# Kernel optimization log

Hardware: AMD Instinct MI355X
Metric: run time of the kernel (lower is better)

## Reference

```python
import jax, jax.numpy as jnp
import numpy as np

M, K, N = 65536, 512, 512
EPS = 1e-05


def setup_inputs() -> dict:
    key = jax.random.key(0)
    k1, k2, k3 = jax.random.split(key, 3)
    x = jax.random.normal(k1, (M, K), dtype=jnp.float32)
    # int8 weight buffer in [-128, 127]
    weight_int8 = jax.random.randint(k2, (N, K), -128, 128, dtype=jnp.int32).astype(jnp.int8)
    # realistic per-output-channel dequant scales (max-abs / 127 of an fp weight)
    weight_scale = jax.random.uniform(k3, (N,), dtype=jnp.float32, minval=0.001, maxval=0.02)
    return {"x": x, "weight_int8": weight_int8, "weight_scale": weight_scale}


def reference(x, weight_int8, weight_scale):
    # dynamic per-tensor quantization of the activation
    x_scale = jnp.maximum(jnp.max(jnp.abs(x)) / 127.0, EPS)
    x_int8 = jnp.clip(jnp.round(x / x_scale), -128, 127).astype(jnp.int8)
    out_int32 = jnp.matmul(x_int8, weight_int8.T, preferred_element_type=jnp.int32)
    # dequantize: per-tensor input scale * per-row weight scale
    out = out_int32.astype(jnp.float32) * (x_scale * weight_scale[None, :])
    return out
```

## Files before the change

### kernel.cpp

```cpp
#include <hip/hip_runtime.h>


#define M_DIM 65536
#define K_DIM 512
#define N_DIM 512
#define EPSF  1e-5f

typedef int int32x4 __attribute__((ext_vector_type(4)));

#define WS_PART   256
#define WS_WPACK  32768

__device__ inline unsigned int pack_w4(int4 v) {
    return (v.x & 0xff) | ((v.y & 0xff) << 8) |
           ((v.z & 0xff) << 16) | ((unsigned)v.w << 24);
}

__device__ inline unsigned int quantpack4(float4 f, float inv) {
    const float C = 12582912.0f;
    unsigned int u0 = __float_as_uint(fmaf(f.x, inv, C));
    unsigned int u1 = __float_as_uint(fmaf(f.y, inv, C));
    unsigned int u2 = __float_as_uint(fmaf(f.z, inv, C));
    unsigned int u3 = __float_as_uint(fmaf(f.w, inv, C));
    unsigned int lo = __builtin_amdgcn_perm(u1, u0, 0x0C0C0400u);
    unsigned int hi = __builtin_amdgcn_perm(u3, u2, 0x04000C0Cu);
    return lo | hi;
}

__global__ void absmax1_pack_kernel(const float* __restrict__ x,
                                    const int* __restrict__ wi,
                                    float* __restrict__ partials,
                                    unsigned int* __restrict__ wp) {
    const int b = blockIdx.x;
    const int t = threadIdx.x;
    if (b < 4096) {
        __shared__ float red[4];
        const float4* x4 = (const float4*)x;
        const int base = b * 2048;
        float m = 0.0f;
        #pragma unroll
        for (int j = 0; j < 8; ++j) {
            float4 v = x4[base + j * 256 + t];
            m = fmaxf(m, fmaxf(fmaxf(fabsf(v.x), fabsf(v.y)),
                               fmaxf(fabsf(v.z), fabsf(v.w))));
        }
        #pragma unroll
        for (int off = 32; off > 0; off >>= 1)
            m = fmaxf(m, __shfl_xor(m, off));
        if ((t & 63) == 0) red[t >> 6] = m;
        __syncthreads();
        if (t == 0)
            partials[b] = fmaxf(fmaxf(red[0], red[1]), fmaxf(red[2], red[3]));
    } else {
        const int bb = b - 4096;
        #pragma unroll
        for (int j = 0; j < 4; ++j) {
            int d = bb * 1024 + j * 256 + t;
            wp[d] = pack_w4(((const int4*)wi)[d]);
        }
    }
}

__global__ __launch_bounds__(256, 4) void quant_gemm_kernel(
    const float* __restrict__ x, const signed char* __restrict__ w,
    const float* __restrict__ wscale, const float* __restrict__ partials,
    float* __restrict__ out) {
    __shared__ __attribute__((aligned(16))) signed char Blds[32 * 1024];
    __shared__ float red[4];

    const int t    = threadIdx.x;
    const int wave = t >> 6;
    const int lane = t & 63;
    const int quad = lane >> 4;
    const int l16  = lane & 15;
    const int m0   = blockIdx.x * 64;
    const int mw   = m0 + wave * 16;

    #pragma unroll
    for (int cc = 0; cc < 2; ++cc) {
        int c = wave * 2 + cc;
        #pragma unroll
        for (int tt = 0; tt < 4; ++tt) {
            const signed char* g = w + (long)(tt * 16 + l16) * K_DIM
                                     + c * 64 + quad * 16;
            __builtin_amdgcn_global_load_lds(
                (const __attribute__((address_space(1))) unsigned int*)g,
                (__attribute__((address_space(3))) unsigned int*)(Blds + (c * 4 + tt) * 1024),
                16, 0, 0);
        }
    }

    float m = 0.0f;
    {
        const float4* p4 = (const float4*)partials;
        #pragma unroll
        for (int j = 0; j < 4; ++j) {
            float4 v = p4[t + j * 256];
            m = fmaxf(m, fmaxf(fmaxf(v.x, v.y), fmaxf(v.z, v.w)));
        }
        #pragma unroll
        for (int off = 32; off > 0; off >>= 1)
            m = fmaxf(m, __shfl_xor(m, off));
        if (lane == 0) red[wave] = m;
    }
    __syncthreads();
    const float mx  = fmaxf(fmaxf(red[0], red[1]), fmaxf(red[2], red[3]));
    const float s   = fmaxf(mx / 127.0f, EPSF);
    const float inv = 1.0f / s;

    int32x4 a[8];
    {
        const float* xr = x + (size_t)(mw + l16) * K_DIM + quad * 16;
        #pragma unroll
        for (int k = 0; k < 8; ++k) {
            float4 v0 = *(const float4*)(xr + k * 64 + 0);
            float4 v1 = *(const float4*)(xr + k * 64 + 4);
            float4 v2 = *(const float4*)(xr + k * 64 + 8);
            float4 v3 = *(const float4*)(xr + k * 64 + 12);
            a[k].x = (int)quantpack4(v0, inv);
            a[k].y = (int)quantpack4(v1, inv);
            a[k].z = (int)quantpack4(v2, inv);
            a[k].w = (int)quantpack4(v3, inv);
        }
    }

    for (int bx = 0; bx < 8; ++bx) {
        const int n0 = bx * 64;
        __syncthreads();

        int32x4 acc[4] = {};
        #pragma unroll
        for (int k = 0; k < 8; ++k) {
            const signed char* bbase = Blds + k * 4096 + lane * 16;
            #pragma unroll
            for (int tt = 0; tt < 4; ++tt) {
                int32x4 bf = *(const int32x4*)(bbase + tt * 1024);
                acc[tt] = __builtin_amdgcn_mfma_i32_16x16x64_i8(a[k], bf, acc[tt], 0, 0, 0);
            }
        }
        __syncthreads();

        if (bx < 7) {
            const int n1 = (bx + 1) * 64;
            #pragma unroll
            for (int cc = 0; cc < 2; ++cc) {
                int c = wave * 2 + cc;
                #pragma unroll
                for (int tt = 0; tt < 4; ++tt) {
                    const signed char* g = w + (long)(n1 + tt * 16 + l16) * K_DIM
                                             + c * 64 + quad * 16;
                    __builtin_amdgcn_global_load_lds(
                        (const __attribute__((address_space(1))) unsigned int*)g,
                        (__attribute__((address_space(3))) unsigned int*)(Blds + (c * 4 + tt) * 1024),
                        16, 0, 0);
                }
            }
        }

        #pragma unroll
        for (int tt = 0; tt < 4; ++tt) {
            int n = n0 + tt * 16 + l16;
            float c = s * wscale[n];
            float* o = out + (long)(mw + quad * 4) * N_DIM + n;
            #pragma unroll
            for (int r = 0; r < 4; ++r)
                o[(long)r * N_DIM] = (float)acc[tt][r] * c;
        }
    }
}

extern "C" void kernel_launch(void* const* d_in, const int* in_sizes, int n_in,
                              void* d_out, int out_size, void* d_ws, size_t ws_size,
                              hipStream_t stream) {
    const float* x   = (const float*)d_in[0];
    const int*   wi  = (const int*)d_in[1];
    const float* sc  = (const float*)d_in[2];
    float*       out = (float*)d_out;

    float*        partials = (float*)((char*)d_ws + WS_PART);
    unsigned int* wp       = (unsigned int*)((char*)d_ws + WS_WPACK);
    const signed char* w8  = (const signed char*)wp;

    absmax1_pack_kernel<<<4160, 256, 0, stream>>>(x, wi, partials, wp);
    quant_gemm_kernel<<<1024, 256, 0, stream>>>(x, w8, sc, partials, out);
}
```

Before: 279.9 us.

## Stage quantized activation tile through swizzled LDS with coalesced x loads

Activation loads become fully contiguous per block: each thread reads 64 consecutive bytes of the 64x512 x tile, quantizes them, and writes int8 into XOR-swizzled LDS. Each wave then reads its MFMA A fragments back from LDS. Before, each lane read 64 bytes from rows strided by 2 KB. The LDS buffer is reused for weights afterward, so the first weight prefetch now starts only after activation staging, losing the overlap it had with the x loads. Two extra barriers are added.

Measured after the change: 274.9 us. About the same (-1.8%).

```diff
diff --git a/kernel.cpp b/kernel.cpp
--- a/kernel.cpp
+++ b/kernel.cpp
@@ -65,7 +65,7 @@
     const float* __restrict__ x, const signed char* __restrict__ w,
     const float* __restrict__ wscale, const float* __restrict__ partials,
     float* __restrict__ out) {
-    __shared__ __attribute__((aligned(16))) signed char Blds[32 * 1024];
+    __shared__ __attribute__((aligned(16))) signed char Lds[32 * 1024];
     __shared__ float red[4];
 
     const int t    = threadIdx.x;
@@ -76,6 +76,58 @@
     const int m0   = blockIdx.x * 64;
     const int mw   = m0 + wave * 16;
 
+    float m = 0.0f;
+    {
+        const float4* p4 = (const float4*)partials;
+        #pragma unroll
+        for (int j = 0; j < 4; ++j) {
+            float4 v = p4[t + j * 256];
+            m = fmaxf(m, fmaxf(fmaxf(v.x, v.y), fmaxf(v.z, v.w)));
+        }
+        #pragma unroll
+        for (int off = 32; off > 0; off >>= 1)
+            m = fmaxf(m, __shfl_xor(m, off));
+        if (lane == 0) red[wave] = m;
+    }
+    __syncthreads();
+    const float mx  = fmaxf(fmaxf(red[0], red[1]), fmaxf(red[2], red[3]));
+    const float s   = fmaxf(mx / 127.0f, EPSF);
+    const float inv = 1.0f / s;
+
+    {
+        const float4* xs = (const float4*)(x + (size_t)m0 * K_DIM);
+        const int rsub = t >> 5;
+        const int csub = (t & 31) * 16;
+        #pragma unroll
+        for (int j = 0; j < 8; ++j) {
+            const int fi = j * 1024 + t * 4;
+            float4 v0 = xs[fi + 0];
+            float4 v1 = xs[fi + 1];
+            float4 v2 = xs[fi + 2];
+            float4 v3 = xs[fi + 3];
+            int32x4 p;
+            p.x = (int)quantpack4(v0, inv);
+            p.y = (int)quantpack4(v1, inv);
+            p.z = (int)quantpack4(v2, inv);
+            p.w = (int)quantpack4(v3, inv);
+            const int row  = j * 8 + rsub;
+            const int addr = (row * 512 + csub) ^ ((row & 7) << 4);
+            *(int32x4*)(Lds + addr) = p;
+        }
+    }
+    __syncthreads();
+
+    int32x4 a[8];
+    {
+        const int r = wave * 16 + l16;
+        #pragma unroll
+        for (int k = 0; k < 8; ++k) {
+            const int c = quad * 16 + k * 64;
+            a[k] = *(const int32x4*)(Lds + ((r * 512 + c) ^ ((r & 7) << 4)));
+        }
+    }
+    __syncthreads();
+
     #pragma unroll
     for (int cc = 0; cc < 2; ++cc) {
         int c = wave * 2 + cc;
@@ -85,42 +137,8 @@
                                      + c * 64 + quad * 16;
             __builtin_amdgcn_global_load_lds(
                 (const __attribute__((address_space(1))) unsigned int*)g,
-                (__attribute__((address_space(3))) unsigned int*)(Blds + (c * 4 + tt) * 1024),
+                (__attribute__((address_space(3))) unsigned int*)(Lds + (c * 4 + tt) * 1024),
                 16, 0, 0);
-        }
-    }
-
-    float m = 0.0f;
-    {
-        const float4* p4 = (const float4*)partials;
-        #pragma unroll
-        for (int j = 0; j < 4; ++j) {
-            float4 v = p4[t + j * 256];
-            m = fmaxf(m, fmaxf(fmaxf(v.x, v.y), fmaxf(v.z, v.w)));
-        }
-        #pragma unroll
-        for (int off = 32; off > 0; off >>= 1)
-            m = fmaxf(m, __shfl_xor(m, off));
-        if (lane == 0) red[wave] = m;
-    }
-    __syncthreads();
-    const float mx  = fmaxf(fmaxf(red[0], red[1]), fmaxf(red[2], red[3]));
-    const float s   = fmaxf(mx / 127.0f, EPSF);
-    const float inv = 1.0f / s;
-
-    int32x4 a[8];
-    {
-        const float* xr = x + (size_t)(mw + l16) * K_DIM + quad * 16;
-        #pragma unroll
-        for (int k = 0; k < 8; ++k) {
-            float4 v0 = *(const float4*)(xr + k * 64 + 0);
-            float4 v1 = *(const float4*)(xr + k * 64 + 4);
-            float4 v2 = *(const float4*)(xr + k * 64 + 8);
-            float4 v3 = *(const float4*)(xr + k * 64 + 12);
-            a[k].x = (int)quantpack4(v0, inv);
-            a[k].y = (int)quantpack4(v1, inv);
-            a[k].z = (int)quantpack4(v2, inv);
-            a[k].w = (int)quantpack4(v3, inv);
         }
     }
 
@@ -131,7 +149,7 @@
         int32x4 acc[4] = {};
         #pragma unroll
         for (int k = 0; k < 8; ++k) {
-            const signed char* bbase = Blds + k * 4096 + lane * 16;
+            const signed char* bbase = Lds + k * 4096 + lane * 16;
             #pragma unroll
             for (int tt = 0; tt < 4; ++tt) {
                 int32x4 bf = *(const int32x4*)(bbase + tt * 1024);
@@ -151,7 +169,7 @@
                                              + c * 64 + quad * 16;
                     __builtin_amdgcn_global_load_lds(
                         (const __attribute__((address_space(1))) unsigned int*)g,
-                        (__attribute__((address_space(3))) unsigned int*)(Blds + (c * 4 + tt) * 1024),
+                        (__attribute__((address_space(3))) unsigned int*)(Lds + (c * 4 + tt) * 1024),
                         16, 0, 0);
                 }
             }
```
